# Performance work log

Measured on AMD Instinct MI355X. Metric: run time of the kernel, lower is better.

Reference implementation:

```python
import jax, jax.numpy as jnp
from jax import lax
import numpy as np

K = 48          # dim_embedding_key
PAST = 20
FUT = 40
N = 65536       # total surrounding-agent nodes
E = 1048576     # edges
B = 1           # batch (structurally forced to 1 by the original code)


def conv1d_relu(x, w, b):
    # x: [B, 2, T], w: [K, 2, 3], padding=1 -> relu(Conv1d)
    y = lax.conv_general_dilated(x, w, (1,), ((1, 1),),
                                 dimension_numbers=('NCH', 'OIH', 'NCH'))
    return jax.nn.relu(y + b[None, :, None])


def gru_cell(xt, h, Wih, Whh, bih, bhh):
    gi = xt @ Wih.T + bih
    gh = h @ Whh.T + bhh
    ir, iz, inn = jnp.split(gi, 3, axis=-1)
    hr, hz, hn = jnp.split(gh, 3, axis=-1)
    r = jax.nn.sigmoid(ir + hr)
    z = jax.nn.sigmoid(iz + hz)
    n = jnp.tanh(inn + r * hn)
    return (1 - z) * n + z * h


def gru_last(x, Wih, Whh, bih, bhh):
    # x: [Nb, T, Din]; returns final hidden state [Nb, H] (torch GRU, h0 = 0)
    h0 = jnp.zeros((x.shape[0], Whh.shape[1]), x.dtype)
    def step(h, xt):
        h2 = gru_cell(xt, h, Wih, Whh, bih, bhh)
        return h2, None
    hT, _ = lax.scan(step, h0, jnp.swapaxes(x, 0, 1))
    return hT


def gcn_conv(x, row, col, w, W, b, n):
    # PyG GCNConv(normalize=True): add self loops (weight 1), symmetric norm,
    # x @ W.T, gather at source `row`, scatter-add at target `col`, + bias.
    loop = jnp.arange(n)
    row = jnp.concatenate([row, loop])
    col = jnp.concatenate([col, loop])
    w = jnp.concatenate([w, jnp.ones((n,), w.dtype)])
    deg = jax.ops.segment_sum(w, col, num_segments=n)
    dinv = jnp.where(deg > 0, lax.rsqrt(jnp.where(deg > 0, deg, 1.0)), 0.0)
    norm = dinv[row] * w * dinv[col]
    xw = x @ W.T
    msg = xw[row] * norm[:, None]
    return jax.ops.segment_sum(msg, col, num_segments=n) + b


def forward(past, future, x, edge_index, edge_weight,
            conv_past_w, conv_past_b, conv_fut_w, conv_fut_b,
            enc_past_Wih, enc_past_Whh, enc_past_bih, enc_past_bhh,
            enc_fut_Wih, enc_fut_Whh, enc_fut_bih, enc_fut_bhh,
            dec_Wih, dec_Whh, dec_bih, dec_bhh,
            fc_w, fc_b, gcn1_w, gcn1_b, gcn2_w, gcn2_b):
    present0 = past[:, -1, :2]                                  # [B, 2]

    # --- surrounding agents: conv1d + GRU encoder over all N nodes ---
    inter_past = jnp.swapaxes(x.reshape(-1, PAST, 2), 1, 2)     # [N, 2, T]
    story_embed = jnp.swapaxes(conv1d_relu(inter_past, conv_past_w, conv_past_b), 1, 2)
    state_past = gru_last(story_embed, enc_past_Wih, enc_past_Whh, enc_past_bih, enc_past_bhh)  # [N, K]

    # --- GCN interaction (edge_weight nonempty branch); dropout is eval-mode identity ---
    ei = edge_index.reshape(2, -1)
    ew = edge_weight.reshape(-1)
    x1 = jax.nn.relu(gcn_conv(state_past, ei[0], ei[1], ew, gcn1_w, gcn1_b, N))
    x1 = gcn_conv(x1, ei[0], ei[1], ew, gcn2_w, gcn2_b, N)
    interact_past = x1[0].reshape(B, -1)                        # [B, K] (B == 1)

    # --- ego past / future encoders ---
    past_embed = jnp.swapaxes(conv1d_relu(jnp.swapaxes(past, 1, 2), conv_past_w, conv_past_b), 1, 2)
    fut_embed = jnp.swapaxes(conv1d_relu(jnp.swapaxes(future, 1, 2), conv_fut_w, conv_fut_b), 1, 2)
    target_past = gru_last(past_embed, enc_past_Wih, enc_past_Whh, enc_past_bih, enc_past_bhh)   # [B, K]
    state_fut = gru_last(fut_embed, enc_fut_Wih, enc_fut_Whh, enc_fut_bih, enc_fut_bhh)          # [B, K]

    state_conc = jnp.concatenate([interact_past, target_past, state_fut], axis=-1)               # [B, 3K]

    zeros_in = jnp.zeros_like(state_conc)
    def step(carry, i):
        h, present = carry
        inp = jnp.where(i == 0, state_conc, zeros_in)
        h = gru_cell(inp, h, dec_Wih, dec_Whh, dec_bih, dec_bhh)
        coords = present + h @ fc_w.T + fc_b
        return (h, coords), coords
    (_, _), coords_seq = lax.scan(step, (jnp.zeros((B, 3 * K), past.dtype), present0), jnp.arange(FUT))
    return jnp.swapaxes(coords_seq, 0, 1)                        # [B, FUT, 2]


def setup_inputs() -> dict:
    ks = jax.random.split(jax.random.key(0), 32)
    def p(k, shape, s=0.1):
        return jax.random.normal(k, shape, jnp.float32) * s
    inp = {
        'past': p(ks[0], (B, PAST, 2), 1.0),
        'future': p(ks[1], (B, FUT, 2), 1.0),
        'x': p(ks[2], (N, PAST, 2), 1.0),
        'edge_index': jax.random.randint(ks[3], (1, 2, E), 0, N, jnp.int32),
        'edge_weight': jax.random.uniform(ks[4], (1, E), jnp.float32),
        'conv_past_w': p(ks[5], (K, 2, 3)), 'conv_past_b': p(ks[6], (K,)),
        'conv_fut_w': p(ks[7], (K, 2, 3)), 'conv_fut_b': p(ks[8], (K,)),
        'enc_past_Wih': p(ks[9], (3 * K, K)), 'enc_past_Whh': p(ks[10], (3 * K, K)),
        'enc_past_bih': p(ks[11], (3 * K,)), 'enc_past_bhh': p(ks[12], (3 * K,)),
        'enc_fut_Wih': p(ks[13], (3 * K, K)), 'enc_fut_Whh': p(ks[14], (3 * K, K)),
        'enc_fut_bih': p(ks[15], (3 * K,)), 'enc_fut_bhh': p(ks[16], (3 * K,)),
        'dec_Wih': p(ks[17], (9 * K, 3 * K)), 'dec_Whh': p(ks[18], (9 * K, 3 * K)),
        'dec_bih': p(ks[19], (9 * K,)), 'dec_bhh': p(ks[20], (9 * K,)),
        'fc_w': p(ks[21], (2, 3 * K)), 'fc_b': p(ks[22], (2,)),
        'gcn1_w': p(ks[23], (K, K)), 'gcn1_b': p(ks[24], (K,)),
        'gcn2_w': p(ks[25], (K, K)), 'gcn2_b': p(ks[26], (K,)),
    }
    return inp


def reference(past, future, x, edge_index, edge_weight,
              conv_past_w, conv_past_b, conv_fut_w, conv_fut_b,
              enc_past_Wih, enc_past_Whh, enc_past_bih, enc_past_bhh,
              enc_fut_Wih, enc_fut_Whh, enc_fut_bih, enc_fut_bhh,
              dec_Wih, dec_Whh, dec_bih, dec_bhh,
              fc_w, fc_b, gcn1_w, gcn1_b, gcn2_w, gcn2_b):
    return forward(past, future, x, edge_index, edge_weight,
                   conv_past_w, conv_past_b, conv_fut_w, conv_fut_b,
                   enc_past_Wih, enc_past_Whh, enc_past_bih, enc_past_bhh,
                   enc_fut_Wih, enc_fut_Whh, enc_fut_bih, enc_fut_bhh,
                   dec_Wih, dec_Whh, dec_bih, dec_bhh,
                   fc_w, fc_b, gcn1_w, gcn1_b, gcn2_w, gcn2_b)
```

## Files before the change

kernel.cpp:

```cpp
#include <hip/hip_runtime.h>
#include <math.h>

#define NN 65536
#define NE 1048576
#define KH 48
#define G3 144
#define DEGB 512
#define PREPB 15
#define E1B 1024
#define SB2 81
#define GIB 2

#define CAP_L1 8192
#define CAP_S1 4096
#define CAP_E2 65536
#define CAP_S2 8192

#define OFF_MARK1  0u
#define OFF_MARK2  262144u
#define OFF_CNT    524288u
#define OFF_L1R    524352u
#define OFF_L1W    557120u
#define OFF_S1G    589888u
#define OFF_E2R    606272u
#define OFF_E2S    868416u
#define OFF_E2W    1130560u
#define OFF_S2     1392704u
#define OFF_DEG2   1425472u
#define OFF_STATE  1458240u
#define OFF_X1     3031104u
#define OFF_TPSF   3817536u
#define OFF_WHH16  3818048u
#define OFF_GI0P   3947072u
#define OFF_GIP    3948800u
#define OFF_GIF    3960320u
#define OFF_DWH4   3983360u

typedef _Float16 h2_t __attribute__((ext_vector_type(2)));
typedef _Float16 h4_t __attribute__((ext_vector_type(4)));
typedef _Float16 h8_t __attribute__((ext_vector_type(8)));

__device__ __forceinline__ float sigmf(float x) { return 1.0f / (1.0f + __expf(-x)); }
__device__ __forceinline__ float tanhfast(float x) {
    float e = __expf(2.0f * x);
    return 1.0f - 2.0f / (e + 1.0f);
}

#if __has_builtin(__builtin_amdgcn_fdot2)
__device__ __forceinline__ float fdot2f(h2_t a, h2_t b, float c) {
    return __builtin_amdgcn_fdot2(a, b, c, false);
}
#else
__device__ __forceinline__ float fdot2f(h2_t a, h2_t b, float c) {
    return c + (float)a.x * (float)b.x + (float)a.y * (float)b.y;
}
#endif

__device__ __forceinline__ void s2_append(int r, unsigned* cnt, int* mark2,
                                          int* s2, float* deg2) {
    if (mark2[r] != 0) return;
    unsigned idx = atomicAdd(&cnt[3], 1u);
    if (idx >= CAP_S2) return;
    int old = atomicCAS(&mark2[r], 0, (int)idx + 1);
    deg2[idx] = 1.0f;
    s2[idx] = (old == 0) ? r : -1;
}

__device__ __forceinline__ void s1_claim(int r, unsigned* cnt, int* mark1,
                                         int* mark2, int* s1g,
                                         int* e2r, int* e2s, float* e2w,
                                         float* x1, const float* g1b,
                                         int* s2, float* deg2) {
    if (mark1[r] != 0) return;
    unsigned idx = atomicAdd(&cnt[1], 1u);
    if (idx >= CAP_S1) return;
    int old = atomicCAS(&mark1[r], 0, (int)idx + 1);
    if (old != 0) return;
    s1g[idx] = r;
    unsigned t2 = atomicAdd(&cnt[2], 1u);
    if (t2 < CAP_E2) { e2r[t2] = r; e2s[t2] = (int)idx; e2w[t2] = 1.0f; }
    for (int k = 0; k < KH; ++k) x1[idx * KH + k] = g1b[k];
    s2_append(r, cnt, mark2, s2, deg2);
}

__global__ void k_edges1(const int* ei, const float* ew,
                         int* mark1, int* mark2, unsigned* cnt,
                         int* l1r, float* l1w, int* s1g,
                         int* e2r, int* e2s, float* e2w,
                         float* x1, const float* g1b, int* s2, float* deg2,
                         const float* past, const float* future,
                         const float* cpw, const float* cpb,
                         const float* cfw, const float* cfb,
                         const float* epWih, const float* epbih,
                         const float* efWih, const float* efbih,
                         float* giP, float* giF) {
    if (blockIdx.x >= E1B) {
        int p = blockIdx.x - E1B;
        const float* xs; const float* cw; const float* cb;
        const float* Wih; const float* bih; float* gout;
        int T, s0;
        if (p < 5) { xs = past;   cw = cpw; cb = cpb; Wih = epWih; bih = epbih;
                     gout = giP; T = 20; s0 = p * 4; }
        else       { xs = future; cw = cfw; cb = cfb; Wih = efWih; bih = efbih;
                     gout = giF; T = 40; s0 = (p - 5) * 4; }
        __shared__ __align__(16) float s_x[80];
        __shared__ __align__(16) float s_e[4 * KH];
        int t = threadIdx.x;
        if (t < T * 2) s_x[t] = xs[t];
        __syncthreads();
        for (int idx = t; idx < 4 * KH; idx += 256) {
            int lt = idx / KH;
            int k = idx - lt * KH;
            int tt = s0 + lt;
            float acc = cb[k];
#pragma unroll
            for (int d = 0; d < 3; ++d) {
                int tau = tt + d - 1;
                if (tau >= 0 && tau < T) {
                    acc += cw[k * 6 + d] * s_x[tau * 2 + 0];
                    acc += cw[k * 6 + 3 + d] * s_x[tau * 2 + 1];
                }
            }
            s_e[lt * KH + k] = fmaxf(acc, 0.0f);
        }
        __syncthreads();
        for (int idx = t; idx < 4 * G3; idx += 256) {
            int lt = idx / G3;
            int row = idx - lt * G3;
            const float4* wp = reinterpret_cast<const float4*>(Wih + row * KH);
            const float4* em = reinterpret_cast<const float4*>(s_e + lt * KH);
            float g = bih[row];
#pragma unroll
            for (int j = 0; j < 12; ++j) {
                float4 w4 = wp[j]; float4 e4 = em[j];
                g += w4.x * e4.x + w4.y * e4.y + w4.z * e4.z + w4.w * e4.w;
            }
            gout[(s0 + lt) * G3 + row] = g;
        }
        return;
    }
    int q = blockIdx.x * blockDim.x + threadIdx.x;
    if (q == 0)
        s1_claim(0, cnt, mark1, mark2, s1g, e2r, e2s, e2w, x1, g1b, s2, deg2);
    int4 c4 = reinterpret_cast<const int4*>(ei + NE)[q];
    int e = q * 4;
    int cc[4] = {c4.x, c4.y, c4.z, c4.w};
#pragma unroll
    for (int j = 0; j < 4; ++j) {
        if (cc[j] == 0) {
            int r = ei[e + j];
            float w = ew[e + j];
            unsigned s = atomicAdd(&cnt[0], 1u);
            if (s < CAP_L1) { l1r[s] = r; l1w[s] = w; }
            s1_claim(r, cnt, mark1, mark2, s1g, e2r, e2s, e2w, x1, g1b, s2, deg2);
        }
    }
}

__global__ void k_edges2(const int* ei, const float* ew,
                         const int* mark1, int* mark2, unsigned* cnt,
                         int* e2r, int* e2s, float* e2w, int* s2, float* deg2,
                         const float* dWhh, const float* dWih,
                         _Float16* whh16, float* dwh4) {
    if (blockIdx.x < SB2) {
        int id = blockIdx.x * blockDim.x + threadIdx.x;
        if (id < 27 * 576) {
            int c = id / 576, t = id - c * 576;
            int k = t >> 2, q = t & 3;
            int g = c / 9, u = c - g * 9;
            const float* src = dWhh + (size_t)(g * G3 + k) * G3 + q * 36 + 4 * u;
            float4 f = *reinterpret_cast<const float4*>(src);
            h2_t a, b;
            a.x = (_Float16)f.x; a.y = (_Float16)f.y;
            b.x = (_Float16)f.z; b.y = (_Float16)f.w;
            int pid = ((c >> 1) * 576 + t) * 2 + (c & 1);
            h2_t* o = reinterpret_cast<h2_t*>(whh16);
            o[2 * pid + 0] = a;
            o[2 * pid + 1] = b;
            return;
        }
        int id2 = id - 27 * 576;
        if (id2 < 9 * 576) {
            int c = id2 / 576, t = id2 - c * 576;
            int k = t >> 2, q = t & 3;
            int g = c / 3, j = c - g * 3;
            const float* src = dWih + (size_t)(g * G3 + k) * G3 + q * 12 + 4 * j;
            reinterpret_cast<float4*>(dwh4)[id2] =
                *reinterpret_cast<const float4*>(src);
        }
        return;
    }
    int q = (blockIdx.x - SB2) * blockDim.x + threadIdx.x;
    if (q >= NE / 4) return;
    int4 c4 = reinterpret_cast<const int4*>(ei + NE)[q];
    int e = q * 4;
    int cc[4] = {c4.x, c4.y, c4.z, c4.w};
#pragma unroll
    for (int j = 0; j < 4; ++j) {
        int m = mark1[cc[j]];
        if (m > 0) {
            int r = ei[e + j];
            float w = ew[e + j];
            unsigned s = atomicAdd(&cnt[2], 1u);
            if (s < CAP_E2) { e2r[s] = r; e2s[s] = m - 1; e2w[s] = w; }
            s2_append(r, cnt, mark2, s2, deg2);
        }
    }
}

__device__ void gru_seq(const float* xseq, int T,
                        const float* cw, const float* cb,
                        const float* Wih, const float* Whh,
                        const float* bih, const float* bhh,
                        float* out48,
                        float* s_x, float* s_embed, float* s_giA,
                        float* s_h ) {
    int t = threadIdx.x;
    int nt = blockDim.x;
    for (int i = t; i < T * 2; i += nt) s_x[i] = xseq[i];
    __syncthreads();
    for (int idx = t; idx < T * KH; idx += nt) {
        int tt = idx / KH;
        int k = idx - tt * KH;
        float acc = cb[k];
#pragma unroll
        for (int d = 0; d < 3; ++d) {
            int tau = tt + d - 1;
            if (tau >= 0 && tau < T) {
                acc += cw[k * 6 + d] * s_x[tau * 2 + 0];
                acc += cw[k * 6 + 3 + d] * s_x[tau * 2 + 1];
            }
        }
        s_embed[tt * KH + k] = fmaxf(acc, 0.0f);
    }
    __syncthreads();
    for (int idx = t; idx < T * G3; idx += nt) {
        int step = idx / G3;
        int row = idx - step * G3;
        const float4* wp = reinterpret_cast<const float4*>(Wih + row * KH);
        const float4* em = reinterpret_cast<const float4*>(s_embed + step * KH);
        float g = bih[row];
#pragma unroll
        for (int j = 0; j < 12; ++j) {
            float4 w4 = wp[j]; float4 e4 = em[j];
            g += w4.x * e4.x + w4.y * e4.y + w4.z * e4.z + w4.w * e4.w;
        }
        s_giA[idx] = g;
    }
    int k = t >> 1, hf = t & 1;
    float4 wr[18];
    float bh0 = 0.0f, bh1 = 0.0f, bh2 = 0.0f;
    if (t < 96) {
#pragma unroll
        for (int g = 0; g < 3; ++g) {
            const float4* q = reinterpret_cast<const float4*>(
                Whh + (g * KH + k) * KH + hf * 24);
#pragma unroll
            for (int j = 0; j < 6; ++j) wr[g * 6 + j] = q[j];
        }
        if (hf == 0) { bh0 = bhh[k]; bh1 = bhh[KH + k]; bh2 = bhh[2 * KH + k]; }
    }
    if (t < KH) s_h[t] = 0.0f;
    float hk = 0.0f;
    for (int step = 0; step < T; ++step) {
        __syncthreads();
        int cur = step & 1, nxt = cur ^ 1;
        if (t < 96) {
            const float4* hp = reinterpret_cast<const float4*>(s_h + cur * KH)
                               + hf * 6;
            float a0 = bh0, a1 = bh1, a2 = bh2;
#pragma unroll
            for (int j = 0; j < 6; ++j) {
                float4 hv = hp[j];
                float4 w0 = wr[j], w1 = wr[6 + j], w2 = wr[12 + j];
                a0 += w0.x * hv.x + w0.y * hv.y + w0.z * hv.z + w0.w * hv.w;
                a1 += w1.x * hv.x + w1.y * hv.y + w1.z * hv.z + w1.w * hv.w;
                a2 += w2.x * hv.x + w2.y * hv.y + w2.z * hv.z + w2.w * hv.w;
            }
            a0 += __shfl_xor(a0, 1);
            a1 += __shfl_xor(a1, 1);
            a2 += __shfl_xor(a2, 1);
            if (hf == 0) {
                const float* gi = s_giA + step * G3;
                float r = sigmf(gi[k] + a0);
                float z = sigmf(gi[KH + k] + a1);
                float n = tanhfast(gi[2 * KH + k] + r * a2);
                hk = (1.0f - z) * n + z * hk;
                s_h[nxt * KH + k] = hk;
            }
        }
    }
    __syncthreads();
    if (t < KH) out48[t] = s_h[(T & 1) * KH + t];
}

__device__ void gru_rec(const float* giA , int T,
                        const float* Whh, const float* bhh,
                        float* out48, float* s_h ) {
    int t = threadIdx.x;
    int k = t >> 1, hf = t & 1;
    float4 wr[18];
    float bh0 = 0.0f, bh1 = 0.0f, bh2 = 0.0f;
    if (t < 96) {
#pragma unroll
        for (int g = 0; g < 3; ++g) {
            const float4* q = reinterpret_cast<const float4*>(
                Whh + (g * KH + k) * KH + hf * 24);
#pragma unroll
            for (int j = 0; j < 6; ++j) wr[g * 6 + j] = q[j];
        }
        if (hf == 0) { bh0 = bhh[k]; bh1 = bhh[KH + k]; bh2 = bhh[2 * KH + k]; }
    }
    if (t < KH) s_h[t] = 0.0f;
    float hk = 0.0f;
    for (int step = 0; step < T; ++step) {
        __syncthreads();
        int cur = step & 1, nxt = cur ^ 1;
        if (t < 96) {
            const float4* hp = reinterpret_cast<const float4*>(s_h + cur * KH)
                               + hf * 6;
            float a0 = bh0, a1 = bh1, a2 = bh2;
#pragma unroll
            for (int j = 0; j < 6; ++j) {
                float4 hv = hp[j];
                float4 w0 = wr[j], w1 = wr[6 + j], w2 = wr[12 + j];
                a0 += w0.x * hv.x + w0.y * hv.y + w0.z * hv.z + w0.w * hv.w;
                a1 += w1.x * hv.x + w1.y * hv.y + w1.z * hv.z + w1.w * hv.w;
                a2 += w2.x * hv.x + w2.y * hv.y + w2.z * hv.z + w2.w * hv.w;
            }
            a0 += __shfl_xor(a0, 1);
            a1 += __shfl_xor(a1, 1);
            a2 += __shfl_xor(a2, 1);
            if (hf == 0) {
                const float* gi = giA + step * G3;
                float r = sigmf(gi[k] + a0);
                float z = sigmf(gi[KH + k] + a1);
                float n = tanhfast(gi[2 * KH + k] + r * a2);
                hk = (1.0f - z) * n + z * hk;
                s_h[nxt * KH + k] = hk;
            }
        }
    }
    __syncthreads();
    if (t < KH) out48[t] = s_h[(T & 1) * KH + t];
}

__global__ __launch_bounds__(192, 2) void k_gru(
    const float* x, const float* cpw, const float* cpb,
    const float* epWih, const float* epWhh, const float* epbih, const float* epbhh,
    const float* efWhh, const float* efbhh,
    const float* giP, const float* giF,
    const int* ei, const float* ew, const int* mark2, float* deg2,
    const int* s2, const unsigned* cnt, float* state, float* tpsf) {
    if (blockIdx.x < DEGB) {
        int per = NE / DEGB;
        int lo = blockIdx.x * per;
        for (int e = lo + threadIdx.x; e < lo + per; e += blockDim.x) {
            int c = ei[NE + e];
            int m = mark2[c];
            if (m > 0) atomicAdd(&deg2[m - 1], ew[e]);
        }
        return;
    }
    __shared__ __align__(16) float s_x[80];
    __shared__ __align__(16) float s_embed[40 * KH];
    __shared__ __align__(16) float s_giA[40 * G3];
    __shared__ __align__(16) float s_h[2 * KH];
    if (blockIdx.x == DEGB) {
        gru_rec(giP, 20, epWhh, epbhh, tpsf, s_h);
        return;
    }
    if (blockIdx.x == DEGB + 1) {
        gru_rec(giF, 40, efWhh, efbhh, tpsf + 64, s_h);
        return;
    }
    int b0 = blockIdx.x - (DEGB + 2);
    int nw = gridDim.x - (DEGB + 2);
    int cnt2 = (int)min(cnt[3], (unsigned)CAP_S2);
    for (int b = b0; b < cnt2; b += nw) {
        int node = s2[b];
        if (node < 0) continue;
        gru_seq(x + (size_t)node * 40, 20, cpw, cpb, epWih, epWhh, epbih, epbhh,
                state + (size_t)b * KH, s_x, s_embed, s_giA, s_h);
    }
}

__global__ void k_acc1(const unsigned* cnt, const int* e2r, const int* e2s,
                       const float* e2w, const int* mark2, const float* deg2,
                       const int* s1g, const float* state,
                       const float* W1, float* x1,
                       const float* dWih, const float* dbih, const float* tpsf,
                       float* gi0p) {
    if (blockIdx.x < GIB) {
        int row = blockIdx.x * blockDim.x + threadIdx.x;
        if (row < 432) {
            const float* wr = dWih + (size_t)row * G3;
            float acc = dbih[row];
#pragma unroll
            for (int m = 0; m < 48; ++m) acc += wr[48 + m] * tpsf[m];
#pragma unroll
            for (int m = 0; m < 48; ++m) acc += wr[96 + m] * tpsf[64 + m];
            gi0p[row] = acc;
        }
        return;
    }
    int nE = (int)min(cnt[2], (unsigned)CAP_E2);
    int total = nE * KH;
    int stride = (gridDim.x - GIB) * blockDim.x;
    for (int idx = (blockIdx.x - GIB) * blockDim.x + threadIdx.x; idx < total;
         idx += stride) {
        int e = idx / KH;
        int k = idx - e * KH;
        int row = e2r[e];
        int s2i = mark2[row] - 1;
        if (s2i < 0) continue;
        int cglob = s1g[e2s[e]];
        int cs2 = mark2[cglob] - 1;
        float norm = e2w[e] * rsqrtf(deg2[s2i] * deg2[cs2]);
        const float* sp = state + (size_t)s2i * KH;
        const float* wp = W1 + k * KH;
        float acc = 0.0f;
#pragma unroll
        for (int m = 0; m < KH; ++m) acc += sp[m] * wp[m];
        atomicAdd(&x1[e2s[e] * KH + k], acc * norm);
    }
}

__global__ __launch_bounds__(640, 1) void k_dec(
    const unsigned* cnt, const int* l1r, const float* l1w,
    const int* mark1, const int* mark2, const float* deg2, const float* x1,
    const float* W2, const float* b2, const float* tpsf, const float* past,
    const _Float16* whh16, const float* dwh4, const float* gi0p,
    const float* dbih, const float* dbhh,
    const float* fcw, const float* fcb, float* out) {
    __shared__ __align__(16) float s_conc[G3];
    __shared__ __align__(16) _Float16 s_h16[2][G3];
    __shared__ __align__(16) float s_hf[2][G3];
    int t = threadIdx.x;
    int k = t >> 2, q = t & 3;
    h8_t wv[13];
    h4_t wv26 = (h4_t)(_Float16)0.0f;
    float4 dv[9];
    float bh[3] = {0.0f, 0.0f, 0.0f};
    float bi[3] = {0.0f, 0.0f, 0.0f};
#pragma unroll
    for (int c2 = 0; c2 < 13; ++c2) wv[c2] = (h8_t)(_Float16)0.0f;
#pragma unroll
    for (int j = 0; j < 9; ++j) dv[j] = make_float4(0.f, 0.f, 0.f, 0.f);
    if (t < 576) {
        const h8_t* wp8 = reinterpret_cast<const h8_t*>(whh16);
#pragma unroll
        for (int c2 = 0; c2 < 13; ++c2) wv[c2] = wp8[c2 * 576 + t];
        wv26 = reinterpret_cast<const h4_t*>(whh16)[(13 * 576 + t) * 2];
        const float4* dp = reinterpret_cast<const float4*>(dwh4);
#pragma unroll
        for (int j = 0; j < 9; ++j) dv[j] = dp[j * 576 + t];
        if (q == 0) {
#pragma unroll
            for (int g = 0; g < 3; ++g) {
                bh[g] = dbhh[g * G3 + k];
                bi[g] = dbih[g * G3 + k];
            }
        }
    }
    float fw0[3] = {0, 0, 0}, fw1[3] = {0, 0, 0};
    float fcb0 = 0.0f, fcb1 = 0.0f, pres0 = 0.0f, pres1 = 0.0f;
    if (t >= 576) {
        int lane = t - 576;
#pragma unroll
        for (int j = 0; j < 3; ++j) {
            int m = lane + 64 * j;
            if (m < G3) { fw0[j] = fcw[m]; fw1[j] = fcw[G3 + m]; }
        }
        if (lane == 0) {
            fcb0 = fcb[0]; fcb1 = fcb[1];
            pres0 = past[38]; pres1 = past[39];
        }
    }
    if (t < 48) s_conc[t] = b2[t];
    else if (t < 96) s_conc[t] = tpsf[t - 48];
    else if (t < 144) s_conc[t] = tpsf[64 + t - 96];
    if (t < G3) {
        s_h16[0][t] = (_Float16)0.0f;
        s_hf[0][t] = 0.0f;
    }
    __syncthreads();
    int cl1 = (int)min(cnt[0], (unsigned)CAP_L1);
    float dinv0 = rsqrtf(deg2[mark2[0] - 1]);
    int items = (cl1 + 1) * KH;
    for (int idx = t; idx < items; idx += blockDim.x) {
        int e = idx / KH;
        int kk = idx - e * KH;
        int row; float norm;
        if (e == cl1) { row = 0; norm = dinv0 * dinv0; }
        else {
            row = l1r[e];
            int rs2 = mark2[row] - 1;
            if (rs2 < 0) continue;
            norm = l1w[e] * rsqrtf(deg2[rs2]) * dinv0;
        }
        int s1 = mark1[row] - 1;
        if (s1 < 0) continue;
        const float* xp = x1 + (size_t)s1 * KH;
        const float* wp = W2 + kk * KH;
        float acc = 0.0f;
#pragma unroll
        for (int m = 0; m < KH; ++m) acc += fmaxf(xp[m], 0.0f) * wp[m];
        atomicAdd(&s_conc[kk], acc * norm);
    }
    h2_t wh[54];
    if (t < 576) {
#pragma unroll
        for (int c2 = 0; c2 < 13; ++c2) {
            h8_t v = wv[c2];
            int c0 = 2 * c2, c1 = 2 * c2 + 1;
            int g0 = c0 / 9, u0 = c0 - g0 * 9;
            int g1 = c1 / 9, u1 = c1 - g1 * 9;
            wh[g0 * 18 + 2 * u0]     = __builtin_shufflevector(v, v, 0, 1);
            wh[g0 * 18 + 2 * u0 + 1] = __builtin_shufflevector(v, v, 2, 3);
            wh[g1 * 18 + 2 * u1]     = __builtin_shufflevector(v, v, 4, 5);
            wh[g1 * 18 + 2 * u1 + 1] = __builtin_shufflevector(v, v, 6, 7);
        }
        wh[2 * 18 + 2 * 8]     = __builtin_shufflevector(wv26, wv26, 0, 1);
        wh[2 * 18 + 2 * 8 + 1] = __builtin_shufflevector(wv26, wv26, 2, 3);
    } else {
#pragma unroll
        for (int j = 0; j < 54; ++j) wh[j] = (h2_t)(_Float16)0.0f;
    }
    __syncthreads();
    float gi0[3] = {0.0f, 0.0f, 0.0f};
    if (t < 576) {
        const float4* cc = reinterpret_cast<const float4*>(s_conc) + q * 3;
        float4 c0 = cc[0], c1 = cc[1], c2v = cc[2];
#pragma unroll
        for (int g = 0; g < 3; ++g) {
            float4 w0 = dv[g * 3 + 0];
            float4 w1 = dv[g * 3 + 1];
            float4 w2 = dv[g * 3 + 2];
            float acc = w0.x * c0.x + w0.y * c0.y + w0.z * c0.z + w0.w * c0.w;
            acc += w1.x * c1.x + w1.y * c1.y + w1.z * c1.z + w1.w * c1.w;
            acc += w2.x * c2v.x + w2.y * c2v.y + w2.z * c2v.z + w2.w * c2v.w;
            acc += __shfl_xor(acc, 1);
            acc += __shfl_xor(acc, 2);
            gi0[g] = acc + gi0p[g * G3 + k];
        }
    }
    float hk = 0.0f;
    for (int i = 0; i < 40; ++i) {
        __syncthreads();
        int cur = i & 1, nxt = cur ^ 1;
        if (t < 576) {
            const h4_t* hp = reinterpret_cast<const h4_t*>(&s_h16[cur][0]) + q * 9;
            float a0 = bh[0], a1 = bh[1], a2 = bh[2];
#pragma unroll
            for (int j = 0; j < 9; ++j) {
                h4_t hv = hp[j];
                h2_t lo = __builtin_shufflevector(hv, hv, 0, 1);
                h2_t hi = __builtin_shufflevector(hv, hv, 2, 3);
                a0 = fdot2f(wh[2 * j], lo, a0);
                a1 = fdot2f(wh[18 + 2 * j], lo, a1);
                a2 = fdot2f(wh[36 + 2 * j], lo, a2);
                a0 = fdot2f(wh[2 * j + 1], hi, a0);
                a1 = fdot2f(wh[18 + 2 * j + 1], hi, a1);
                a2 = fdot2f(wh[36 + 2 * j + 1], hi, a2);
            }
            a0 += __shfl_xor(a0, 1); a0 += __shfl_xor(a0, 2);
            a1 += __shfl_xor(a1, 1); a1 += __shfl_xor(a1, 2);
            a2 += __shfl_xor(a2, 1); a2 += __shfl_xor(a2, 2);
            if (q == 0) {
                float gr = ((i == 0) ? gi0[0] : bi[0]) + a0;
                float gz = ((i == 0) ? gi0[1] : bi[1]) + a1;
                float gn = ((i == 0) ? gi0[2] : bi[2]);
                float r = sigmf(gr);
                float z = sigmf(gz);
                float n = tanhfast(gn + r * a2);
                hk = (1.0f - z) * n + z * hk;
                s_h16[nxt][k] = (_Float16)hk;
                s_hf[nxt][k] = hk;
            }
        } else if (i >= 1) {
            int lane = t - 576;
            const float* hsrc = s_hf[cur];
            float p0 = 0.0f, p1 = 0.0f;
#pragma unroll
            for (int j = 0; j < 3; ++j) {
                int m = lane + 64 * j;
                if (m < G3) { float h = hsrc[m]; p0 += h * fw0[j]; p1 += h * fw1[j]; }
            }
#pragma unroll
            for (int off = 32; off > 0; off >>= 1) {
                p0 += __shfl_down(p0, off);
                p1 += __shfl_down(p1, off);
            }
            if (lane == 0) {
                pres0 += p0 + fcb0; pres1 += p1 + fcb1;
                out[(i - 1) * 2 + 0] = pres0;
                out[(i - 1) * 2 + 1] = pres1;
            }
        }
    }
    __syncthreads();
    if (t >= 576) {
        int lane = t - 576;
        const float* hsrc = s_hf[0];
        float p0 = 0.0f, p1 = 0.0f;
#pragma unroll
        for (int j = 0; j < 3; ++j) {
            int m = lane + 64 * j;
            if (m < G3) { float h = hsrc[m]; p0 += h * fw0[j]; p1 += h * fw1[j]; }
        }
#pragma unroll
        for (int off = 32; off > 0; off >>= 1) {
            p0 += __shfl_down(p0, off);
            p1 += __shfl_down(p1, off);
        }
        if (lane == 0) {
            pres0 += p0 + fcb0; pres1 += p1 + fcb1;
            out[39 * 2 + 0] = pres0;
            out[39 * 2 + 1] = pres1;
        }
    }
}

extern "C" void kernel_launch(void* const* d_in, const int* in_sizes, int n_in,
                              void* d_out, int out_size, void* d_ws, size_t ws_size,
                              hipStream_t stream) {
    (void)in_sizes; (void)n_in; (void)out_size; (void)ws_size;
    const float* past   = (const float*)d_in[0];
    const float* future = (const float*)d_in[1];
    const float* x      = (const float*)d_in[2];
    const int*   ei     = (const int*)d_in[3];
    const float* ew     = (const float*)d_in[4];
    const float* cpw    = (const float*)d_in[5];
    const float* cpb    = (const float*)d_in[6];
    const float* cfw    = (const float*)d_in[7];
    const float* cfb    = (const float*)d_in[8];
    const float* epWih  = (const float*)d_in[9];
    const float* epWhh  = (const float*)d_in[10];
    const float* epbih  = (const float*)d_in[11];
    const float* epbhh  = (const float*)d_in[12];
    const float* efWih  = (const float*)d_in[13];
    const float* efWhh  = (const float*)d_in[14];
    const float* efbih  = (const float*)d_in[15];
    const float* efbhh  = (const float*)d_in[16];
    const float* dWih   = (const float*)d_in[17];
    const float* dWhh   = (const float*)d_in[18];
    const float* dbih   = (const float*)d_in[19];
    const float* dbhh   = (const float*)d_in[20];
    const float* fcw    = (const float*)d_in[21];
    const float* fcb    = (const float*)d_in[22];
    const float* g1w    = (const float*)d_in[23];
    const float* g1b    = (const float*)d_in[24];
    const float* g2w    = (const float*)d_in[25];
    const float* g2b    = (const float*)d_in[26];

    char* ws = (char*)d_ws;
    int*      mark1 = (int*)(ws + OFF_MARK1);
    int*      mark2 = (int*)(ws + OFF_MARK2);
    unsigned* cnt   = (unsigned*)(ws + OFF_CNT);
    int*      l1r   = (int*)(ws + OFF_L1R);
    float*    l1w   = (float*)(ws + OFF_L1W);
    int*      s1g   = (int*)(ws + OFF_S1G);
    int*      e2r   = (int*)(ws + OFF_E2R);
    int*      e2s   = (int*)(ws + OFF_E2S);
    float*    e2w   = (float*)(ws + OFF_E2W);
    int*      s2    = (int*)(ws + OFF_S2);
    float*    deg2  = (float*)(ws + OFF_DEG2);
    float*    state = (float*)(ws + OFF_STATE);
    float*    x1    = (float*)(ws + OFF_X1);
    float*    tpsf  = (float*)(ws + OFF_TPSF);
    _Float16* whh16 = (_Float16*)(ws + OFF_WHH16);
    float*    gi0p  = (float*)(ws + OFF_GI0P);
    float*    giP   = (float*)(ws + OFF_GIP);
    float*    giF   = (float*)(ws + OFF_GIF);
    float*    dwh4  = (float*)(ws + OFF_DWH4);

    hipMemsetAsync(ws, 0, 524352, stream);
    k_edges1<<<E1B + PREPB, 256, 0, stream>>>(
        ei, ew, mark1, mark2, cnt, l1r, l1w, s1g, e2r, e2s, e2w,
        x1, g1b, s2, deg2,
        past, future, cpw, cpb, cfw, cfb,
        epWih, epbih, efWih, efbih, giP, giF);
    k_edges2<<<SB2 + E1B, 256, 0, stream>>>(ei, ew, mark1, mark2, cnt,
                                            e2r, e2s, e2w, s2, deg2,
                                            dWhh, dWih, whh16, dwh4);
    k_gru<<<DEGB + 2 + 512, 192, 0, stream>>>(x, cpw, cpb, epWih, epWhh, epbih, epbhh,
                                              efWhh, efbhh, giP, giF,
                                              ei, ew, mark2, deg2,
                                              s2, cnt, state, tpsf);
    k_acc1<<<GIB + 128, 256, 0, stream>>>(cnt, e2r, e2s, e2w, mark2, deg2, s1g,
                                          state, g1w, x1,
                                          dWih, dbih, tpsf, gi0p);
    k_dec<<<1, 640, 0, stream>>>(cnt, l1r, l1w, mark1, mark2, deg2, x1, g2w, g2b,
                                 tpsf, past, whh16, dwh4, gi0p, dbih, dbhh, fcw, fcb,
                                 (float*)d_out);
}
```

Before: 212.4 us.

## Split decoder GRU hidden dot products across 2 lanes instead of 4

The single-block decoder kernel now assigns each hidden unit to 2 threads rather than 4, so each thread holds 72 fp16 recurrent weights and 72 input weights in registers. The block shrinks from 640 to 384 threads, one cross-lane shuffle stage per reduction is removed, and the weight-repacking kernel is changed to match the new layout. The goal is a shorter serial 40-step recurrence, at the cost of more register pressure and longer per-thread dot products.

```diff
diff --git a/kernel.cpp b/kernel.cpp
--- a/kernel.cpp
+++ b/kernel.cpp
@@ -164,27 +164,26 @@
                          _Float16* whh16, float* dwh4) {
     if (blockIdx.x < SB2) {
         int id = blockIdx.x * blockDim.x + threadIdx.x;
-        if (id < 27 * 576) {
-            int c = id / 576, t = id - c * 576;
-            int k = t >> 2, q = t & 3;
+        if (id < 27 * 288 * 2) {
+            int pid = id >> 1, half = id & 1;
+            int c = pid / 288, t = pid - c * 288;
+            int k = t >> 1, hf = t & 1;
             int g = c / 9, u = c - g * 9;
-            const float* src = dWhh + (size_t)(g * G3 + k) * G3 + q * 36 + 4 * u;
+            const float* src = dWhh + (size_t)(g * G3 + k) * G3
+                               + hf * 72 + 8 * u + 4 * half;
             float4 f = *reinterpret_cast<const float4*>(src);
-            h2_t a, b;
-            a.x = (_Float16)f.x; a.y = (_Float16)f.y;
-            b.x = (_Float16)f.z; b.y = (_Float16)f.w;
-            int pid = ((c >> 1) * 576 + t) * 2 + (c & 1);
-            h2_t* o = reinterpret_cast<h2_t*>(whh16);
-            o[2 * pid + 0] = a;
-            o[2 * pid + 1] = b;
+            h4_t o;
+            o.x = (_Float16)f.x; o.y = (_Float16)f.y;
+            o.z = (_Float16)f.z; o.w = (_Float16)f.w;
+            reinterpret_cast<h4_t*>(whh16)[2 * pid + half] = o;
             return;
         }
-        int id2 = id - 27 * 576;
-        if (id2 < 9 * 576) {
-            int c = id2 / 576, t = id2 - c * 576;
-            int k = t >> 2, q = t & 3;
-            int g = c / 3, j = c - g * 3;
-            const float* src = dWih + (size_t)(g * G3 + k) * G3 + q * 12 + 4 * j;
+        int id2 = id - 27 * 288 * 2;
+        if (id2 < 18 * 288) {
+            int c = id2 / 288, t = id2 - c * 288;
+            int k = t >> 1, hf = t & 1;
+            int g = c / 6, j = c - g * 6;
+            const float* src = dWih + (size_t)(g * G3 + k) * G3 + hf * 24 + 4 * j;
             reinterpret_cast<float4*>(dwh4)[id2] =
                 *reinterpret_cast<const float4*>(src);
         }
@@ -426,7 +425,7 @@
     }
 }
 
-__global__ __launch_bounds__(640, 1) void k_dec(
+__global__ __launch_bounds__(384, 1) void k_dec(
     const unsigned* cnt, const int* l1r, const float* l1w,
     const int* mark1, const int* mark2, const float* deg2, const float* x1,
     const float* W2, const float* b2, const float* tpsf, const float* past,
@@ -437,25 +436,23 @@
     __shared__ __align__(16) _Float16 s_h16[2][G3];
     __shared__ __align__(16) float s_hf[2][G3];
     int t = threadIdx.x;
-    int k = t >> 2, q = t & 3;
-    h8_t wv[13];
-    h4_t wv26 = (h4_t)(_Float16)0.0f;
-    float4 dv[9];
+    int k = t >> 1, hf = t & 1;
+    h8_t wv[27];
+    float4 dv[18];
     float bh[3] = {0.0f, 0.0f, 0.0f};
     float bi[3] = {0.0f, 0.0f, 0.0f};
 #pragma unroll
-    for (int c2 = 0; c2 < 13; ++c2) wv[c2] = (h8_t)(_Float16)0.0f;
-#pragma unroll
-    for (int j = 0; j < 9; ++j) dv[j] = make_float4(0.f, 0.f, 0.f, 0.f);
-    if (t < 576) {
+    for (int c = 0; c < 27; ++c) wv[c] = (h8_t)(_Float16)0.0f;
+#pragma unroll
+    for (int c = 0; c < 18; ++c) dv[c] = make_float4(0.f, 0.f, 0.f, 0.f);
+    if (t < 288) {
         const h8_t* wp8 = reinterpret_cast<const h8_t*>(whh16);
 #pragma unroll
-        for (int c2 = 0; c2 < 13; ++c2) wv[c2] = wp8[c2 * 576 + t];
-        wv26 = reinterpret_cast<const h4_t*>(whh16)[(13 * 576 + t) * 2];
+        for (int c = 0; c < 27; ++c) wv[c] = wp8[c * 288 + t];
         const float4* dp = reinterpret_cast<const float4*>(dwh4);
 #pragma unroll
-        for (int j = 0; j < 9; ++j) dv[j] = dp[j * 576 + t];
-        if (q == 0) {
+        for (int c = 0; c < 18; ++c) dv[c] = dp[c * 288 + t];
+        if (hf == 0) {
 #pragma unroll
             for (int g = 0; g < 3; ++g) {
                 bh[g] = dbhh[g * G3 + k];
@@ -465,8 +462,8 @@
     }
     float fw0[3] = {0, 0, 0}, fw1[3] = {0, 0, 0};
     float fcb0 = 0.0f, fcb1 = 0.0f, pres0 = 0.0f, pres1 = 0.0f;
-    if (t >= 576) {
-        int lane = t - 576;
+    if (t >= 320) {
+        int lane = t - 320;
 #pragma unroll
         for (int j = 0; j < 3; ++j) {
             int m = lane + 64 * j;
@@ -508,40 +505,23 @@
         for (int m = 0; m < KH; ++m) acc += fmaxf(xp[m], 0.0f) * wp[m];
         atomicAdd(&s_conc[kk], acc * norm);
     }
-    h2_t wh[54];
-    if (t < 576) {
-#pragma unroll
-        for (int c2 = 0; c2 < 13; ++c2) {
-            h8_t v = wv[c2];
-            int c0 = 2 * c2, c1 = 2 * c2 + 1;
-            int g0 = c0 / 9, u0 = c0 - g0 * 9;
-            int g1 = c1 / 9, u1 = c1 - g1 * 9;
-            wh[g0 * 18 + 2 * u0]     = __builtin_shufflevector(v, v, 0, 1);
-            wh[g0 * 18 + 2 * u0 + 1] = __builtin_shufflevector(v, v, 2, 3);
-            wh[g1 * 18 + 2 * u1]     = __builtin_shufflevector(v, v, 4, 5);
-            wh[g1 * 18 + 2 * u1 + 1] = __builtin_shufflevector(v, v, 6, 7);
-        }
-        wh[2 * 18 + 2 * 8]     = __builtin_shufflevector(wv26, wv26, 0, 1);
-        wh[2 * 18 + 2 * 8 + 1] = __builtin_shufflevector(wv26, wv26, 2, 3);
-    } else {
-#pragma unroll
-        for (int j = 0; j < 54; ++j) wh[j] = (h2_t)(_Float16)0.0f;
-    }
     __syncthreads();
     float gi0[3] = {0.0f, 0.0f, 0.0f};
-    if (t < 576) {
-        const float4* cc = reinterpret_cast<const float4*>(s_conc) + q * 3;
-        float4 c0 = cc[0], c1 = cc[1], c2v = cc[2];
+    if (t < 288) {
+        const float4* ccp = reinterpret_cast<const float4*>(s_conc) + hf * 6;
+        float4 c0 = ccp[0], c1 = ccp[1], c2 = ccp[2];
+        float4 c3 = ccp[3], c4 = ccp[4], c5 = ccp[5];
 #pragma unroll
         for (int g = 0; g < 3; ++g) {
-            float4 w0 = dv[g * 3 + 0];
-            float4 w1 = dv[g * 3 + 1];
-            float4 w2 = dv[g * 3 + 2];
+            float4 w0 = dv[g * 6 + 0], w1 = dv[g * 6 + 1], w2 = dv[g * 6 + 2];
+            float4 w3 = dv[g * 6 + 3], w4 = dv[g * 6 + 4], w5 = dv[g * 6 + 5];
             float acc = w0.x * c0.x + w0.y * c0.y + w0.z * c0.z + w0.w * c0.w;
             acc += w1.x * c1.x + w1.y * c1.y + w1.z * c1.z + w1.w * c1.w;
-            acc += w2.x * c2v.x + w2.y * c2v.y + w2.z * c2v.z + w2.w * c2v.w;
+            acc += w2.x * c2.x + w2.y * c2.y + w2.z * c2.z + w2.w * c2.w;
+            acc += w3.x * c3.x + w3.y * c3.y + w3.z * c3.z + w3.w * c3.w;
+            acc += w4.x * c4.x + w4.y * c4.y + w4.z * c4.z + w4.w * c4.w;
+            acc += w5.x * c5.x + w5.y * c5.y + w5.z * c5.z + w5.w * c5.w;
             acc += __shfl_xor(acc, 1);
-            acc += __shfl_xor(acc, 2);
             gi0[g] = acc + gi0p[g * G3 + k];
         }
     }
@@ -549,25 +529,34 @@
     for (int i = 0; i < 40; ++i) {
         __syncthreads();
         int cur = i & 1, nxt = cur ^ 1;
-        if (t < 576) {
-            const h4_t* hp = reinterpret_cast<const h4_t*>(&s_h16[cur][0]) + q * 9;
+        if (t < 288) {
+            const h8_t* hp = reinterpret_cast<const h8_t*>(&s_h16[cur][0]) + hf * 9;
             float a0 = bh[0], a1 = bh[1], a2 = bh[2];
 #pragma unroll
             for (int j = 0; j < 9; ++j) {
-                h4_t hv = hp[j];
-                h2_t lo = __builtin_shufflevector(hv, hv, 0, 1);
-                h2_t hi = __builtin_shufflevector(hv, hv, 2, 3);
-                a0 = fdot2f(wh[2 * j], lo, a0);
-                a1 = fdot2f(wh[18 + 2 * j], lo, a1);
-                a2 = fdot2f(wh[36 + 2 * j], lo, a2);
-                a0 = fdot2f(wh[2 * j + 1], hi, a0);
-                a1 = fdot2f(wh[18 + 2 * j + 1], hi, a1);
-                a2 = fdot2f(wh[36 + 2 * j + 1], hi, a2);
-            }
-            a0 += __shfl_xor(a0, 1); a0 += __shfl_xor(a0, 2);
-            a1 += __shfl_xor(a1, 1); a1 += __shfl_xor(a1, 2);
-            a2 += __shfl_xor(a2, 1); a2 += __shfl_xor(a2, 2);
-            if (q == 0) {
+                h8_t hv = hp[j];
+                h2_t h0 = __builtin_shufflevector(hv, hv, 0, 1);
+                h2_t h1 = __builtin_shufflevector(hv, hv, 2, 3);
+                h2_t h2v = __builtin_shufflevector(hv, hv, 4, 5);
+                h2_t h3 = __builtin_shufflevector(hv, hv, 6, 7);
+                h8_t w0v = wv[j], w1v = wv[9 + j], w2v = wv[18 + j];
+                a0 = fdot2f(__builtin_shufflevector(w0v, w0v, 0, 1), h0, a0);
+                a1 = fdot2f(__builtin_shufflevector(w1v, w1v, 0, 1), h0, a1);
+                a2 = fdot2f(__builtin_shufflevector(w2v, w2v, 0, 1), h0, a2);
+                a0 = fdot2f(__builtin_shufflevector(w0v, w0v, 2, 3), h1, a0);
+                a1 = fdot2f(__builtin_shufflevector(w1v, w1v, 2, 3), h1, a1);
+                a2 = fdot2f(__builtin_shufflevector(w2v, w2v, 2, 3), h1, a2);
+                a0 = fdot2f(__builtin_shufflevector(w0v, w0v, 4, 5), h2v, a0);
+                a1 = fdot2f(__builtin_shufflevector(w1v, w1v, 4, 5), h2v, a1);
+                a2 = fdot2f(__builtin_shufflevector(w2v, w2v, 4, 5), h2v, a2);
+                a0 = fdot2f(__builtin_shufflevector(w0v, w0v, 6, 7), h3, a0);
+                a1 = fdot2f(__builtin_shufflevector(w1v, w1v, 6, 7), h3, a1);
+                a2 = fdot2f(__builtin_shufflevector(w2v, w2v, 6, 7), h3, a2);
+            }
+            a0 += __shfl_xor(a0, 1);
+            a1 += __shfl_xor(a1, 1);
+            a2 += __shfl_xor(a2, 1);
+            if (hf == 0) {
                 float gr = ((i == 0) ? gi0[0] : bi[0]) + a0;
                 float gz = ((i == 0) ? gi0[1] : bi[1]) + a1;
                 float gn = ((i == 0) ? gi0[2] : bi[2]);
@@ -578,8 +567,8 @@
                 s_h16[nxt][k] = (_Float16)hk;
                 s_hf[nxt][k] = hk;
             }
-        } else if (i >= 1) {
-            int lane = t - 576;
+        } else if (t >= 320 && i >= 1) {
+            int lane = t - 320;
             const float* hsrc = s_hf[cur];
             float p0 = 0.0f, p1 = 0.0f;
 #pragma unroll
@@ -600,8 +589,8 @@
         }
     }
     __syncthreads();
-    if (t >= 576) {
-        int lane = t - 576;
+    if (t >= 320) {
+        int lane = t - 320;
         const float* hsrc = s_hf[0];
         float p0 = 0.0f, p1 = 0.0f;
 #pragma unroll
@@ -691,7 +680,7 @@
     k_acc1<<<GIB + 128, 256, 0, stream>>>(cnt, e2r, e2s, e2w, mark2, deg2, s1g,
                                           state, g1w, x1,
                                           dWih, dbih, tpsf, gi0p);
-    k_dec<<<1, 640, 0, stream>>>(cnt, l1r, l1w, mark1, mark2, deg2, x1, g2w, g2b,
+    k_dec<<<1, 384, 0, stream>>>(cnt, l1r, l1w, mark1, mark2, deg2, x1, g2w, g2b,
                                  tpsf, past, whh16, dwh4, gi0p, dbih, dbhh, fcw, fcb,
                                  (float*)d_out);
 }
```

Measured after the change: 208.0 us, median of 2. 1.02x faster.
